# Optimization experiments

Measured on AMD Instinct MI355X. Metric: run time of the kernel, lower is better.

Reference implementation:

```python
import jax, jax.numpy as jnp
import numpy as np
from jax import lax


def setup_inputs() -> dict:
    key = jax.random.key(0)
    k1, k2, k3 = jax.random.split(key, 3)
    B, C, H, W = 32, 256, 64, 64
    x = jax.random.normal(k1, (B, C, H, W), dtype=jnp.float32)
    # ECA conv1d: 1 in-ch, 1 out-ch, kernel 5 (derived from C=256), no bias
    conv1d_w = jax.random.normal(k2, (1, 1, 5), dtype=jnp.float32) * 0.3
    # Spatial conv2d: 2 in-ch, 1 out-ch, kernel 7, with bias
    conv2d_w = jax.random.normal(k3, (1, 2, 7, 7), dtype=jnp.float32) * 0.1
    conv2d_b = jnp.zeros((1,), dtype=jnp.float32)
    return {"x": x, "conv1d_w": conv1d_w, "conv2d_w": conv2d_w, "conv2d_b": conv2d_b}


def reference(x, conv1d_w, conv2d_w, conv2d_b):
    # --- ECA channel attention ---
    # global avg pool over H,W -> [B, C]
    y = jnp.mean(x, axis=(2, 3))
    # conv1d across the channel axis (treated as length), 1 feature channel
    y = y[:, None, :]  # [B, 1, C]
    y = lax.conv_general_dilated(
        y, conv1d_w, window_strides=(1,), padding=[(2, 2)],
        dimension_numbers=("NCH", "OIH", "NCH"))
    ch_w = jax.nn.sigmoid(y)[:, 0, :, None, None]  # [B, C, 1, 1]
    eca_out = x * ch_w

    # --- spatial attention ---
    max_pool = jnp.max(x, axis=1, keepdims=True)   # [B,1,H,W]
    avg_pool = jnp.mean(x, axis=1, keepdims=True)  # [B,1,H,W]
    sp_in = jnp.concatenate([max_pool, avg_pool], axis=1)  # [B,2,H,W]
    sp = lax.conv_general_dilated(
        sp_in, conv2d_w, window_strides=(1, 1), padding=[(3, 3), (3, 3)],
        dimension_numbers=("NCHW", "OIHW", "NCHW"))
    sp = jax.nn.sigmoid(sp + conv2d_b[None, :, None, None])  # [B,1,H,W]

    return eca_out + x * sp + x
```

## Files before the change

kernel.cpp:

```cpp
#include <hip/hip_runtime.h>
#include <math.h>

#define BB 32
#define CC 256
#define HH 64
#define WW 64
#define HWSZ (HH * WW)
#define NCHUNK 16

__global__ __launch_bounds__(256, 2) void stats_kernel(
    const float* __restrict__ x, float* __restrict__ chan_part,
    float* __restrict__ pool_max, float* __restrict__ pool_sum) {
  const int b = blockIdx.x >> 4;
  const int chunk = blockIdx.x & 15;
  const int hw0 = chunk << 8;
  const int tid = threadIdx.x;
  const int wave = tid >> 6;
  const int lane = tid & 63;
  const int c_base = wave << 6;

  const float4* xp =
      (const float4*)(x + ((size_t)b << 20) + ((size_t)c_base << 12) + hw0) + lane;

  float4 mx = make_float4(-3.4e38f, -3.4e38f, -3.4e38f, -3.4e38f);
  float4 sm = make_float4(0.f, 0.f, 0.f, 0.f);

  for (int g = 0; g < 4; ++g) {
    float s[16];
#pragma unroll
    for (int ci = 0; ci < 16; ++ci) {
      const float4 v = xp[(g * 16 + ci) * (HWSZ / 4)];
      mx.x = fmaxf(mx.x, v.x); mx.y = fmaxf(mx.y, v.y);
      mx.z = fmaxf(mx.z, v.z); mx.w = fmaxf(mx.w, v.w);
      sm.x += v.x; sm.y += v.y; sm.z += v.z; sm.w += v.w;
      s[ci] = (v.x + v.y) + (v.z + v.w);
    }
#pragma unroll
    for (int ci = 0; ci < 16; ++ci) {
      float v = s[ci];
#pragma unroll
      for (int off = 32; off > 0; off >>= 1) v += __shfl_xor(v, off, 64);
      s[ci] = v;
    }
    if (lane == 0) {
      float4* cp = (float4*)(chan_part +
                             ((size_t)(b * NCHUNK + chunk)) * CC + c_base + g * 16);
      cp[0] = make_float4(s[0],  s[1],  s[2],  s[3]);
      cp[1] = make_float4(s[4],  s[5],  s[6],  s[7]);
      cp[2] = make_float4(s[8],  s[9],  s[10], s[11]);
      cp[3] = make_float4(s[12], s[13], s[14], s[15]);
    }
  }

  __shared__ float4 lmax[4][64];
  __shared__ float4 lsum[4][64];
  lmax[wave][lane] = mx;
  lsum[wave][lane] = sm;
  __syncthreads();
  if (tid < 64) {
    const float4 a = lmax[0][tid], b4 = lmax[1][tid];
    const float4 c4 = lmax[2][tid], d4 = lmax[3][tid];
    float4 M;
    M.x = fmaxf(fmaxf(a.x, b4.x), fmaxf(c4.x, d4.x));
    M.y = fmaxf(fmaxf(a.y, b4.y), fmaxf(c4.y, d4.y));
    M.z = fmaxf(fmaxf(a.z, b4.z), fmaxf(c4.z, d4.z));
    M.w = fmaxf(fmaxf(a.w, b4.w), fmaxf(c4.w, d4.w));
    const float4 sa = lsum[0][tid], sb = lsum[1][tid];
    const float4 sc = lsum[2][tid], sd = lsum[3][tid];
    float4 S;
    S.x = (sa.x + sb.x) + (sc.x + sd.x);
    S.y = (sa.y + sb.y) + (sc.y + sd.y);
    S.z = (sa.z + sb.z) + (sc.z + sd.z);
    S.w = (sa.w + sb.w) + (sc.w + sd.w);
    ((float4*)(pool_max + ((size_t)b << 12) + hw0))[tid] = M;
    ((float4*)(pool_sum + ((size_t)b << 12) + hw0))[tid] = S;
  }
}

__global__ __launch_bounds__(256) void eca_kernel(
    const float* __restrict__ chan_part, const float* __restrict__ w5,
    float* __restrict__ ch_w) {
  __shared__ float m[CC];
  const int b = blockIdx.x;
  const int c = threadIdx.x;
  float s = 0.0f;
#pragma unroll
  for (int k = 0; k < NCHUNK; ++k) s += chan_part[(size_t)(b * NCHUNK + k) * CC + c];
  m[c] = s * (1.0f / HWSZ);
  __syncthreads();

  float acc = 0.0f;
#pragma unroll
  for (int k = 0; k < 5; ++k) {
    int cc = c + k - 2;
    float v = (cc >= 0 && cc < CC) ? m[cc] : 0.0f;
    acc = fmaf(v, w5[k], acc);
  }
  ch_w[b * CC + c] = 1.0f / (1.0f + __expf(-acc));
}

__global__ __launch_bounds__(256) void spatial_kernel(
    const float* __restrict__ pool_max, const float* __restrict__ pool_sum,
    const float* __restrict__ w2, const float* __restrict__ bias,
    float* __restrict__ sp) {
  const int idx = blockIdx.x * 256 + threadIdx.x;
  const int b = idx >> 12;
  const int hw = idx & (HWSZ - 1);
  const int h = hw >> 6;
  const int w = hw & 63;

  float acc = bias[0];
#pragma unroll
  for (int kh = 0; kh < 7; ++kh) {
    const int hh = h + kh - 3;
    if (hh < 0 || hh >= HH) continue;
#pragma unroll
    for (int kw = 0; kw < 7; ++kw) {
      const int ww = w + kw - 3;
      if (ww < 0 || ww >= WW) continue;
      const int off = b * HWSZ + hh * WW + ww;
      acc = fmaf(pool_max[off], w2[kh * 7 + kw], acc);
      acc = fmaf(pool_sum[off], w2[49 + kh * 7 + kw] * (1.0f / CC), acc);
    }
  }
  sp[idx] = 1.0f / (1.0f + __expf(-acc));
}

__global__ __launch_bounds__(256) void combine_kernel(
    const float* __restrict__ x, const float* __restrict__ ch_w,
    const float* __restrict__ sp, float* __restrict__ out) {
  const size_t f = (size_t)blockIdx.x * 256 + threadIdx.x;
  const size_t e = f * 4;
  const int b = (int)(e >> 20);
  const int c = (int)(e >> 12) & 255;
  const int hw = (int)e & (HWSZ - 1);

  const float4 x4 = ((const float4*)x)[f];
  const float4 s4 = ((const float4*)(sp + ((size_t)b << 12)))[hw >> 2];
  const float cw = ch_w[b * CC + c] + 1.0f;

  float4 o;
  o.x = x4.x * (cw + s4.x);
  o.y = x4.y * (cw + s4.y);
  o.z = x4.z * (cw + s4.z);
  o.w = x4.w * (cw + s4.w);
  ((float4*)out)[f] = o;
}

extern "C" void kernel_launch(void* const* d_in, const int* in_sizes, int n_in,
                              void* d_out, int out_size, void* d_ws, size_t ws_size,
                              hipStream_t stream) {
  const float* x    = (const float*)d_in[0];
  const float* w1   = (const float*)d_in[1];
  const float* w2   = (const float*)d_in[2];
  const float* bias = (const float*)d_in[3];
  float* out = (float*)d_out;

  float* ws = (float*)d_ws;
  float* chan_part = ws;
  float* ch_w      = ws + 131072;
  float* pool_max  = ws + 139264;
  float* pool_sum  = ws + 270336;
  float* sp        = ws + 401408;

  stats_kernel<<<BB * NCHUNK, 256, 0, stream>>>(x, chan_part, pool_max, pool_sum);
  eca_kernel<<<BB, 256, 0, stream>>>(chan_part, w1, ch_w);
  spatial_kernel<<<(BB * HWSZ) / 256, 256, 0, stream>>>(pool_max, pool_sum, w2, bias, sp);
  combine_kernel<<<(BB * CC * HWSZ) / (4 * 256), 256, 0, stream>>>(x, ch_w, sp, out);
}
```

Measured before the change: 259.3 us.

## Use LDS transpose for channel sums, merge ECA/spatial kernels, nontemporal output stores

The stats kernel now writes per-lane partial channel sums into shared memory and reduces them with a transposed read, replacing 16 wave-wide shuffle reductions per group. The ECA and spatial-conv kernels are merged into one launch to save a kernel boundary. The combine kernel indexes by block per channel plane and writes output with nontemporal stores to avoid polluting cache. In exchange the stats kernel uses about 70KB more LDS, which may lower occupancy.

After: 260.2 us. About the same (+0.4%).

```diff
diff --git a/kernel.cpp b/kernel.cpp
--- a/kernel.cpp
+++ b/kernel.cpp
@@ -7,6 +7,8 @@
 #define WW 64
 #define HWSZ (HH * WW)
 #define NCHUNK 16
+
+typedef float f32x4 __attribute__((ext_vector_type(4)));
 
 __global__ __launch_bounds__(256, 2) void stats_kernel(
     const float* __restrict__ x, float* __restrict__ chan_part,
@@ -18,6 +20,10 @@
   const int wave = tid >> 6;
   const int lane = tid & 63;
   const int c_base = wave << 6;
+
+  __shared__ float cs[4][64][68];
+  __shared__ float4 lmax[4][64];
+  __shared__ float4 lsum[4][64];
 
   const float4* xp =
       (const float4*)(x + ((size_t)b << 20) + ((size_t)c_base << 12) + hw0) + lane;
@@ -35,27 +41,29 @@
       sm.x += v.x; sm.y += v.y; sm.z += v.z; sm.w += v.w;
       s[ci] = (v.x + v.y) + (v.z + v.w);
     }
-#pragma unroll
-    for (int ci = 0; ci < 16; ++ci) {
-      float v = s[ci];
-#pragma unroll
-      for (int off = 32; off > 0; off >>= 1) v += __shfl_xor(v, off, 64);
-      s[ci] = v;
-    }
-    if (lane == 0) {
-      float4* cp = (float4*)(chan_part +
-                             ((size_t)(b * NCHUNK + chunk)) * CC + c_base + g * 16);
-      cp[0] = make_float4(s[0],  s[1],  s[2],  s[3]);
-      cp[1] = make_float4(s[4],  s[5],  s[6],  s[7]);
-      cp[2] = make_float4(s[8],  s[9],  s[10], s[11]);
-      cp[3] = make_float4(s[12], s[13], s[14], s[15]);
-    }
+    float4* dst = (float4*)&cs[wave][lane][g * 16];
+    dst[0] = make_float4(s[0],  s[1],  s[2],  s[3]);
+    dst[1] = make_float4(s[4],  s[5],  s[6],  s[7]);
+    dst[2] = make_float4(s[8],  s[9],  s[10], s[11]);
+    dst[3] = make_float4(s[12], s[13], s[14], s[15]);
   }
 
-  __shared__ float4 lmax[4][64];
-  __shared__ float4 lsum[4][64];
   lmax[wave][lane] = mx;
   lsum[wave][lane] = sm;
+
+  {
+    float t0 = 0.f, t1 = 0.f, t2 = 0.f, t3 = 0.f;
+#pragma unroll
+    for (int j = 0; j < 64; j += 4) {
+      t0 += cs[wave][j + 0][lane];
+      t1 += cs[wave][j + 1][lane];
+      t2 += cs[wave][j + 2][lane];
+      t3 += cs[wave][j + 3][lane];
+    }
+    chan_part[((size_t)(b * NCHUNK + chunk)) * CC + c_base + lane] =
+        (t0 + t1) + (t2 + t3);
+  }
+
   __syncthreads();
   if (tid < 64) {
     const float4 a = lmax[0][tid], b4 = lmax[1][tid];
@@ -77,74 +85,76 @@
   }
 }
 
-__global__ __launch_bounds__(256) void eca_kernel(
+__global__ __launch_bounds__(256) void attn_kernel(
     const float* __restrict__ chan_part, const float* __restrict__ w5,
-    float* __restrict__ ch_w) {
-  __shared__ float m[CC];
-  const int b = blockIdx.x;
-  const int c = threadIdx.x;
-  float s = 0.0f;
-#pragma unroll
-  for (int k = 0; k < NCHUNK; ++k) s += chan_part[(size_t)(b * NCHUNK + k) * CC + c];
-  m[c] = s * (1.0f / HWSZ);
-  __syncthreads();
-
-  float acc = 0.0f;
-#pragma unroll
-  for (int k = 0; k < 5; ++k) {
-    int cc = c + k - 2;
-    float v = (cc >= 0 && cc < CC) ? m[cc] : 0.0f;
-    acc = fmaf(v, w5[k], acc);
-  }
-  ch_w[b * CC + c] = 1.0f / (1.0f + __expf(-acc));
-}
-
-__global__ __launch_bounds__(256) void spatial_kernel(
+    float* __restrict__ ch_w,
     const float* __restrict__ pool_max, const float* __restrict__ pool_sum,
     const float* __restrict__ w2, const float* __restrict__ bias,
     float* __restrict__ sp) {
-  const int idx = blockIdx.x * 256 + threadIdx.x;
-  const int b = idx >> 12;
-  const int hw = idx & (HWSZ - 1);
-  const int h = hw >> 6;
-  const int w = hw & 63;
+  if (blockIdx.x < BB) {
+    __shared__ float m[CC];
+    const int b = blockIdx.x;
+    const int c = threadIdx.x;
+    float s = 0.0f;
+#pragma unroll
+    for (int k = 0; k < NCHUNK; ++k)
+      s += chan_part[(size_t)(b * NCHUNK + k) * CC + c];
+    m[c] = s * (1.0f / HWSZ);
+    __syncthreads();
 
-  float acc = bias[0];
+    float acc = 0.0f;
 #pragma unroll
-  for (int kh = 0; kh < 7; ++kh) {
-    const int hh = h + kh - 3;
-    if (hh < 0 || hh >= HH) continue;
+    for (int k = 0; k < 5; ++k) {
+      int cc = c + k - 2;
+      float v = (cc >= 0 && cc < CC) ? m[cc] : 0.0f;
+      acc = fmaf(v, w5[k], acc);
+    }
+    ch_w[b * CC + c] = 1.0f / (1.0f + __expf(-acc));
+  } else {
+    const int idx = (blockIdx.x - BB) * 256 + threadIdx.x;
+    const int b = idx >> 12;
+    const int hw = idx & (HWSZ - 1);
+    const int h = hw >> 6;
+    const int w = hw & 63;
+
+    float acc = bias[0];
 #pragma unroll
-    for (int kw = 0; kw < 7; ++kw) {
-      const int ww = w + kw - 3;
-      if (ww < 0 || ww >= WW) continue;
-      const int off = b * HWSZ + hh * WW + ww;
-      acc = fmaf(pool_max[off], w2[kh * 7 + kw], acc);
-      acc = fmaf(pool_sum[off], w2[49 + kh * 7 + kw] * (1.0f / CC), acc);
+    for (int kh = 0; kh < 7; ++kh) {
+      const int hh = h + kh - 3;
+      if (hh < 0 || hh >= HH) continue;
+#pragma unroll
+      for (int kw = 0; kw < 7; ++kw) {
+        const int ww = w + kw - 3;
+        if (ww < 0 || ww >= WW) continue;
+        const int off = b * HWSZ + hh * WW + ww;
+        acc = fmaf(pool_max[off], w2[kh * 7 + kw], acc);
+        acc = fmaf(pool_sum[off], w2[49 + kh * 7 + kw] * (1.0f / CC), acc);
+      }
     }
+    sp[idx] = 1.0f / (1.0f + __expf(-acc));
   }
-  sp[idx] = 1.0f / (1.0f + __expf(-acc));
 }
 
 __global__ __launch_bounds__(256) void combine_kernel(
     const float* __restrict__ x, const float* __restrict__ ch_w,
     const float* __restrict__ sp, float* __restrict__ out) {
-  const size_t f = (size_t)blockIdx.x * 256 + threadIdx.x;
-  const size_t e = f * 4;
-  const int b = (int)(e >> 20);
-  const int c = (int)(e >> 12) & 255;
-  const int hw = (int)e & (HWSZ - 1);
+  const int blk = blockIdx.x;
+  const int b = blk >> 10;
+  const int c = (blk >> 2) & 255;
+  const int hw0 = (blk & 3) << 10;
+  const int t4 = threadIdx.x;
 
-  const float4 x4 = ((const float4*)x)[f];
-  const float4 s4 = ((const float4*)(sp + ((size_t)b << 12)))[hw >> 2];
-  const float cw = ch_w[b * CC + c] + 1.0f;
+  const float cw = 1.0f + ch_w[b * CC + c];
+  const size_t plane = ((size_t)b << 20) + ((size_t)c << 12) + hw0;
+  const float4 x4 = ((const float4*)(x + plane))[t4];
+  const float4 s4 = ((const float4*)(sp + ((size_t)b << 12) + hw0))[t4];
 
-  float4 o;
+  f32x4 o;
   o.x = x4.x * (cw + s4.x);
   o.y = x4.y * (cw + s4.y);
   o.z = x4.z * (cw + s4.z);
   o.w = x4.w * (cw + s4.w);
-  ((float4*)out)[f] = o;
+  __builtin_nontemporal_store(o, (f32x4*)(out + plane) + t4);
 }
 
 extern "C" void kernel_launch(void* const* d_in, const int* in_sizes, int n_in,
@@ -164,7 +174,7 @@
   float* sp        = ws + 401408;
 
   stats_kernel<<<BB * NCHUNK, 256, 0, stream>>>(x, chan_part, pool_max, pool_sum);
-  eca_kernel<<<BB, 256, 0, stream>>>(chan_part, w1, ch_w);
-  spatial_kernel<<<(BB * HWSZ) / 256, 256, 0, stream>>>(pool_max, pool_sum, w2, bias, sp);
+  attn_kernel<<<BB + (BB * HWSZ) / 256, 256, 0, stream>>>(
+      chan_part, w1, ch_w, pool_max, pool_sum, w2, bias, sp);
   combine_kernel<<<(BB * CC * HWSZ) / (4 * 256), 256, 0, stream>>>(x, ch_w, sp, out);
 }
```
